# Performance work log

Hardware: AMD Instinct MI355X
Metric: run time of the kernel (lower is better)

## Reference

```python
import jax, jax.numpy as jnp
import numpy as np

B, O, N = 8, 100, 4096
TOK_D, D, K, H = 2048, 256, 128, 8
DH = D // H
LN_EPS = 1e-5


def _ln(x, g, b):
    m = x.mean(-1, keepdims=True)
    v = ((x - m) ** 2).mean(-1, keepdims=True)
    return (x - m) * jax.lax.rsqrt(v + LN_EPS) * g + b


def setup_inputs() -> dict:
    key = jax.random.key(0)
    ks = jax.random.split(key, 16)
    s = 0.02
    return {
        "activation": jax.random.uniform(ks[0], (B, O, N), jnp.float32),
        "tokens": jax.random.normal(ks[1], (B, N, TOK_D), jnp.float32),
        "W_tok": jax.random.normal(ks[2], (TOK_D, D), jnp.float32) * s,
        "b_tok": jnp.zeros((D,), jnp.float32),
        "g_tn": jnp.ones((D,), jnp.float32),
        "bt_tn": jnp.zeros((D,), jnp.float32),
        "pool_query": jax.random.normal(ks[3], (D,), jnp.float32) * s,
        "Wq": jax.random.normal(ks[4], (D, D), jnp.float32) * s,
        "bq": jnp.zeros((D,), jnp.float32),
        "Wk": jax.random.normal(ks[5], (D, D), jnp.float32) * s,
        "bk": jnp.zeros((D,), jnp.float32),
        "Wv": jax.random.normal(ks[6], (D, D), jnp.float32) * s,
        "bv": jnp.zeros((D,), jnp.float32),
        "Wo": jax.random.normal(ks[7], (D, D), jnp.float32) * s,
        "bo": jnp.zeros((D,), jnp.float32),
        "g_pn": jnp.ones((D,), jnp.float32),
        "bt_pn": jnp.zeros((D,), jnp.float32),
        "g_on": jnp.ones((D,), jnp.float32),
        "bt_on": jnp.zeros((D,), jnp.float32),
    }


def reference(activation, tokens, W_tok, b_tok, g_tn, bt_tn, pool_query,
              Wq, bq, Wk, bk, Wv, bv, Wo, bo, g_pn, bt_pn, g_on, bt_on):
    # project + norm the shared token pool: [B, N, D]
    tp = _ln(tokens @ W_tok + b_tok, g_tn, bt_tn)

    # weighted-average branch
    w = activation / jnp.clip(activation.sum(-1, keepdims=True), 1e-8)
    weighted_avg = jnp.einsum('bon,bnd->bod', w, tp)

    # top-k attention branch
    _, topk_idx = jax.lax.top_k(activation, K)            # [B, O, K]
    topk_tokens = jax.vmap(lambda t, i: t[i])(tp, topk_idx)  # [B, O, K, D]

    # MultiheadAttention with a single shared query vector (q_len = 1)
    q = (pool_query @ Wq + bq).reshape(H, DH)             # [H, DH]
    kp = (topk_tokens @ Wk + bk).reshape(B, O, K, H, DH)
    vp = (topk_tokens @ Wv + bv).reshape(B, O, K, H, DH)
    scores = jnp.einsum('hd,bokhd->bohk', q, kp) / np.sqrt(DH).astype(np.float32)
    attn = jax.nn.softmax(scores, axis=-1)                # [B, O, H, K]
    pooled = jnp.einsum('bohk,bokhd->bohd', attn, vp).reshape(B, O, D)
    pooled = _ln(pooled @ Wo + bo, g_pn, bt_pn)

    return _ln(weighted_avg + pooled, g_on, bt_on)
```

## Files before the change

### kernel.cpp

```cpp
#include <hip/hip_runtime.h>
#include <hip/hip_bf16.h>

#define DEVI static __device__ __forceinline__

typedef __attribute__((ext_vector_type(8))) short short8;
typedef __attribute__((ext_vector_type(4))) float f32x4;

#define B_   8
#define O_   100
#define N_   4096
#define TOKD 2048
#define D_   256
#define K_   128
#define H_   8
#define M_   (B_*N_)

DEVI unsigned short f2bf(float f) {
    unsigned u = __float_as_uint(f);
    u = (u + 0x7FFFu + ((u >> 16) & 1u)) >> 16;
    return (unsigned short)u;
}
DEVI float bf2f(unsigned v) { return __uint_as_float(v << 16); }

DEVI unsigned pkbf(float lo, float hi) {
    unsigned r;
    asm("v_cvt_pk_bf16_f32 %0, %1, %2" : "=v"(r) : "v"(lo), "v"(hi));
    return r;
}
DEVI void gload16(const void* g, void* l) {
    __builtin_amdgcn_global_load_lds((const __attribute__((address_space(1))) void*)g,
                                     (__attribute__((address_space(3))) void*)l, 16, 0, 0);
}

__global__ __launch_bounds__(256) void k_pre(const float* __restrict__ act,
                                             int* __restrict__ oidx,
                                             float* __restrict__ asum,
                                             const float* __restrict__ W,
                                             unsigned short* __restrict__ wtb,
                                             const float* __restrict__ pq,
                                             const float* __restrict__ Wq,
                                             const float* __restrict__ bqv,
                                             const float* __restrict__ Wk,
                                             const float* __restrict__ bkv,
                                             float* __restrict__ qW,
                                             float* __restrict__ qb) {
    __shared__ __align__(16) char smem[50304];
    const int t = threadIdx.x, lane = t & 63, wid = t >> 6;

    if (blockIdx.x >= 800) {
        const int bx = blockIdx.x - 800;
        if (bx < 2048) {
            int idx = bx * 256 + t;
            int k = idx >> 8, n = idx & 255;
            wtb[n * TOKD + k] = f2bf(W[idx]);
            return;
        }
        float (*qpart)[32] = (float(*)[32])smem;
        float* qhl = (float*)(smem + 1024);
        const int h = bx - 2048;
        const int col = h * 32 + (t & 31), sl = t >> 5;
        float s = 0.f;
        #pragma unroll
        for (int e = 0; e < 32; ++e) s += pq[sl * 32 + e] * Wq[(sl * 32 + e) * D_ + col];
        qpart[sl][t & 31] = s;
        __syncthreads();
        if (t < 32) {
            float u = bqv[h * 32 + t];
            #pragma unroll
            for (int s8 = 0; s8 < 8; ++s8) u += qpart[s8][t];
            qhl[t] = u;
        }
        __syncthreads();
        float u = 0.f;
        #pragma unroll
        for (int dd = 0; dd < 32; ++dd) u += qhl[dd] * Wk[t * D_ + h * 32 + dd];
        qW[h * D_ + t] = u;
        if (t == 0) {
            float z = 0.f;
            for (int dd = 0; dd < 32; ++dd) z += qhl[dd] * bkv[h * 32 + dd];
            qb[h] = z;
        }
        return;
    }

    int* hist = (int*)smem;
    unsigned long long* cand = (unsigned long long*)(smem + 16384);
    int* csum = (int*)(smem + 49152);
    int* sb   = (int*)(smem + 50192);
    int* cnts = (int*)(smem + 50200);
    float* redf = (float*)(smem + 50208);
    unsigned long long* redu = (unsigned long long*)(smem + 50224);

    const int blk = blockIdx.x;
    const float* rp = act + (size_t)blk * N_;
    float fv[16]; unsigned vb[16]; int bins[16];
    float fs = 0.f;
    #pragma unroll
    for (int i = 0; i < 16; ++i) {
        float f = rp[t + i * 256];
        fv[i] = f; vb[i] = __float_as_uint(f);
        fs += f;
    }
    #pragma unroll
    for (int i = 0; i < 16; ++i) hist[t + i * 256] = 0;
    if (t == 0) { cnts[0] = 0; cnts[1] = 0; }
    #pragma unroll
    for (int m = 1; m < 64; m <<= 1) fs += __shfl_xor(fs, m);
    if (!lane) redf[wid] = fs;
    __syncthreads();
    if (t == 0) asum[blk] = fmaxf(redf[0] + redf[1] + redf[2] + redf[3], 1e-8f);

    #pragma unroll
    for (int i = 0; i < 16; ++i) {
        float f = fv[i];
        int b = (f >= 1.0f) ? 4095 : ((f > 0.f) ? (int)(f * 4096.f) : 0);
        bins[i] = b;
        atomicAdd(&hist[b], 1);
    }
    __syncthreads();

    int cs = 0;
    #pragma unroll
    for (int i = 0; i < 16; ++i) cs += hist[t * 16 + i];
    int v = cs;
    #pragma unroll
    for (int off = 1; off < 64; off <<= 1) {
        int o = __shfl_down(v, off);
        if (lane + off < 64) v += o;
    }
    if (!lane) csum[256 + wid] = v;
    __syncthreads();
    int stot = 0;
    for (int w2 = wid + 1; w2 < 4; ++w2) stot += csum[256 + w2];
    int suff = v + stot;
    csum[t] = suff;
    __syncthreads();
    int nxtc = (t < 255) ? csum[t + 1] : 0;
    if (suff >= K_ && nxtc < K_) {
        int run = nxtc, bstar = t * 16;
        for (int bi = 15; bi >= 0; --bi) {
            run += hist[t * 16 + bi];
            if (run >= K_) { bstar = t * 16 + bi; break; }
        }
        sb[0] = bstar;
    }
    __syncthreads();
    const int bstar = sb[0];

    #pragma unroll
    for (int i = 0; i < 16; ++i) {
        if (bins[i] > bstar) {
            int p = atomicAdd(&cnts[0], 1);
            oidx[blk * K_ + p] = t + i * 256;
        } else if (bins[i] == bstar) {
            int p = atomicAdd(&cnts[1], 1);
            cand[p] = ((unsigned long long)vb[i] << 16) | (unsigned)(4095 - (t + i * 256));
        }
    }
    __syncthreads();
    const int g = cnts[0], E = cnts[1], m = K_ - g;
    unsigned long long last = ~0ull;
    for (int slot = 0; slot < m; ++slot) {
        unsigned long long best = 0;
        for (int i = t; i < E; i += 256) {
            unsigned long long e = cand[i];
            if (e < last && e > best) best = e;
        }
        #pragma unroll
        for (int mm = 1; mm < 64; mm <<= 1) {
            unsigned long long o = __shfl_xor(best, mm);
            if (o > best) best = o;
        }
        if (!lane) redu[wid] = best;
        __syncthreads();
        best = redu[0];
        if (redu[1] > best) best = redu[1];
        if (redu[2] > best) best = redu[2];
        if (redu[3] > best) best = redu[3];
        if (t == 0) oidx[blk * K_ + g + slot] = 4095 - (int)(best & 0xFFFFull);
        last = best;
        __syncthreads();
    }
}

__global__ __launch_bounds__(512, 2) void k_gemm1(const float* __restrict__ A,
                                                  const unsigned short* __restrict__ Bt,
                                                  const float* __restrict__ btok,
                                                  const float* __restrict__ g,
                                                  const float* __restrict__ bt,
                                                  unsigned short* __restrict__ tp) {
    __shared__ __align__(16) char smem[81920];
    const int t = threadIdx.x;
    const int bm = blockIdx.x;
    const int lane = t & 63, w = t >> 6;
    const int wm = w >> 2, wn = w & 3;
    const int lr = lane >> 4, lc = lane & 15;

    const int arow = t >> 3;
    const int acb = (t & 7) * 16;
    const float* agp = A + (size_t)(bm * 64 + arow) * TOKD + (t & 7) * 8;
    const int aw0 = arow * 128 + (acb ^ ((arow & 7) << 4));
    const unsigned short* bg = Bt + (size_t)(t >> 3) * TOKD
                        + (((((t & 7) << 4)) ^ (((t >> 3) & 7) << 4)) >> 1);
    char* bld = smem + 16384 + (w << 10);

    f32x4 acc[2][4] = {};
    const int NT = TOKD / 64;
    float4 a0, a1;

    a0 = *(const float4*)(agp); a1 = *(const float4*)(agp + 4);
    #pragma unroll
    for (int c = 0; c < 4; ++c) gload16(bg + (size_t)c * 64 * TOKD, bld + c * 8192);
    {
        uint4 v;
        v.x = pkbf(a0.x, a0.y); v.y = pkbf(a0.z, a0.w);
        v.z = pkbf(a1.x, a1.y); v.w = pkbf(a1.z, a1.w);
        *(uint4*)(smem + aw0) = v;
    }
    a0 = *(const float4*)(agp + 64); a1 = *(const float4*)(agp + 68);
    asm volatile("s_waitcnt vmcnt(2) lgkmcnt(0)" ::: "memory");
    __builtin_amdgcn_s_barrier();

    int cur = 0;
    for (int kt = 0; kt < NT; ++kt) {
        const int nxt = cur ^ 1;
        if (kt + 1 < NT) {
            const unsigned short* bn = bg + (size_t)(kt + 1) * 64;
            char* dst = bld + nxt * 32768;
            #pragma unroll
            for (int c = 0; c < 4; ++c) gload16(bn + (size_t)c * 64 * TOKD, dst + c * 8192);
        }
        const char* Ab = smem + cur * 8192;
        const char* Bb = smem + 16384 + cur * 32768;
        #pragma unroll
        for (int kk = 0; kk < 2; ++kk) {
            short8 afr[2], bfr[4];
            #pragma unroll
            for (int mi = 0; mi < 2; ++mi) {
                int row = wm * 32 + mi * 16 + lc;
                afr[mi] = *(const short8*)(Ab + row * 128 + ((kk * 64 + lr * 16) ^ ((row & 7) << 4)));
            }
            #pragma unroll
            for (int ni = 0; ni < 4; ++ni) {
                int n = wn * 64 + ni * 16 + lc;
                bfr[ni] = *(const short8*)(Bb + n * 128 + ((kk * 64 + lr * 16) ^ ((n & 7) << 4)));
            }
            __builtin_amdgcn_s_setprio(1);
            #pragma unroll
            for (int mi = 0; mi < 2; ++mi)
                #pragma unroll
                for (int ni = 0; ni < 4; ++ni)
                    acc[mi][ni] = __builtin_amdgcn_mfma_f32_16x16x32_bf16(afr[mi], bfr[ni], acc[mi][ni], 0, 0, 0);
            __builtin_amdgcn_s_setprio(0);
        }
        if (kt + 1 < NT) {
            uint4 v;
            v.x = pkbf(a0.x, a0.y); v.y = pkbf(a0.z, a0.w);
            v.z = pkbf(a1.x, a1.y); v.w = pkbf(a1.z, a1.w);
            *(uint4*)(smem + nxt * 8192 + aw0) = v;
            if (kt + 2 < NT) {
                const float* ap = agp + (size_t)(kt + 2) * 64;
                a0 = *(const float4*)(ap); a1 = *(const float4*)(ap + 4);
                asm volatile("s_waitcnt vmcnt(2) lgkmcnt(0)" ::: "memory");
            } else {
                asm volatile("s_waitcnt vmcnt(0) lgkmcnt(0)" ::: "memory");
            }
            __builtin_amdgcn_s_barrier();
            cur = nxt;
        }
    }
    __syncthreads();

    float* ep = (float*)smem;
    const int col0 = lane * 4;
    float4 b4 = *(const float4*)(btok + col0);
    float4 g4 = *(const float4*)(g + col0);
    float4 t4 = *(const float4*)(bt + col0);
    #pragma unroll
    for (int c = 0; c < 2; ++c) {
        if (wm == c) {
            #pragma unroll
            for (int mi = 0; mi < 2; ++mi)
                #pragma unroll
                for (int ni = 0; ni < 4; ++ni)
                    #pragma unroll
                    for (int r = 0; r < 4; ++r)
                        ep[(mi * 16 + lr * 4 + r) * 260 + wn * 64 + ni * 16 + lc] = acc[mi][ni][r];
        }
        __syncthreads();
        #pragma unroll
        for (int rr = 0; rr < 4; ++rr) {
            int row = w * 4 + rr;
            float4 x4 = *(const float4*)(ep + row * 260 + col0);
            float x0 = x4.x + b4.x, x1 = x4.y + b4.y, x2 = x4.z + b4.z, x3 = x4.w + b4.w;
            float s = x0 + x1 + x2 + x3;
            float q = x0*x0 + x1*x1 + x2*x2 + x3*x3;
            #pragma unroll
            for (int m = 1; m < 64; m <<= 1) { s += __shfl_xor(s, m); q += __shfl_xor(q, m); }
            float mean = s * (1.f/256.f);
            float var = q * (1.f/256.f) - mean * mean;
            float rs = rsqrtf(var + 1e-5f);
            ushort4 o;
            o.x = f2bf((x0-mean)*rs*g4.x + t4.x);
            o.y = f2bf((x1-mean)*rs*g4.y + t4.y);
            o.z = f2bf((x2-mean)*rs*g4.z + t4.z);
            o.w = f2bf((x3-mean)*rs*g4.w + t4.w);
            *(ushort4*)(tp + (size_t)(bm * 64 + c * 32 + row) * D_ + col0) = o;
        }
        __syncthreads();
    }
}

__global__ __launch_bounds__(256) void k_wavg(const float* __restrict__ act,
                                              const unsigned short* __restrict__ tp,
                                              float* __restrict__ partial) {
    const int kc = blockIdx.x;
    const int b = blockIdx.y;
    const int d = threadIdx.x;
    const unsigned short* tpb = tp + ((size_t)b * N_ + kc * 128) * D_ + d;
    const float* actb = act + (size_t)b * O_ * N_ + kc * 128;
    float* pout = partial + ((size_t)(b * 32 + kc) * O_) * D_ + d;
    for (int oci = 0; oci < 2; ++oci) {
        const int oc = blockIdx.z * 2 + oci;
        float acc[10] = {};
        #pragma unroll 2
        for (int q = 0; q < 32; ++q) {
            float t0 = bf2f(tpb[(q * 4 + 0) * D_]);
            float t1 = bf2f(tpb[(q * 4 + 1) * D_]);
            float t2 = bf2f(tpb[(q * 4 + 2) * D_]);
            float t3 = bf2f(tpb[(q * 4 + 3) * D_]);
            #pragma unroll
            for (int oj = 0; oj < 10; ++oj) {
                float4 a4 = *(const float4*)(actb + (size_t)(oc * 10 + oj) * N_ + q * 4);
                acc[oj] += a4.x * t0 + a4.y * t1 + a4.z * t2 + a4.w * t3;
            }
        }
        #pragma unroll
        for (int oj = 0; oj < 10; ++oj)
            pout[(size_t)(oc * 10 + oj) * D_] = acc[oj];
    }
}

DEVI int swz(int j, int chunk) { return j * 512 + ((chunk ^ (j & 31)) << 4); }

__global__ __launch_bounds__(256) void k_attn(
    const unsigned short* __restrict__ tp, const int* __restrict__ oidx,
    const float* __restrict__ qW, const float* __restrict__ qbv,
    const float* __restrict__ Wv, const float* __restrict__ bv,
    const float* __restrict__ Wo, const float* __restrict__ bo,
    const float* __restrict__ g_pn, const float* __restrict__ bt_pn,
    const float* __restrict__ g_on, const float* __restrict__ bt_on,
    const float* __restrict__ partial, const float* __restrict__ asum,
    float* __restrict__ outp)
{
    __shared__ uint4 tgU[4096];
    __shared__ float sc[H_ * K_];
    __shared__ float ul[H_ * D_];
    __shared__ float pool_lds[D_];
    __shared__ float redf[8];
    __shared__ int idxl[K_];
    char* tg = (char*)tgU;

    const int t = threadIdx.x, lane = t & 63, wid = t >> 6;
    const int blk = blockIdx.x;
    const int b = blk / O_;
    const int o = blk - b * O_;

    if (t < K_) idxl[t] = oidx[blk * K_ + t];
    __syncthreads();

    #pragma unroll
    for (int it = 0; it < 16; ++it) {
        int c = t + it * 256;
        int j = c >> 5, ch = c & 31;
        uint4 v = *(const uint4*)(tp + ((size_t)(b * N_ + idxl[j])) * D_ + ch * 8);
        *(uint4*)(tg + swz(j, ch)) = v;
    }
    __syncthreads();

    {
        const int j = t & 127, hq = t >> 7;
        const float* q0 = qW + hq * 4 * D_;
        float s0 = 0.f, s1 = 0.f, s2 = 0.f, s3 = 0.f;
        #pragma unroll 4
        for (int e8 = 0; e8 < 32; ++e8) {
            uint4 tv = *(const uint4*)(tg + swz(j, e8));
            float f0 = bf2f(tv.x & 0xffffu), f1 = bf2f(tv.x >> 16);
            float f2 = bf2f(tv.y & 0xffffu), f3 = bf2f(tv.y >> 16);
            float f4 = bf2f(tv.z & 0xffffu), f5 = bf2f(tv.z >> 16);
            float f6 = bf2f(tv.w & 0xffffu), f7 = bf2f(tv.w >> 16);
            const float* qa = q0 + e8 * 8;
            const float* qbp = qa + D_;
            const float* qc = qa + 2 * D_;
            const float* qd = qa + 3 * D_;
            s0 += f0*qa[0]+f1*qa[1]+f2*qa[2]+f3*qa[3]+f4*qa[4]+f5*qa[5]+f6*qa[6]+f7*qa[7];
            s1 += f0*qbp[0]+f1*qbp[1]+f2*qbp[2]+f3*qbp[3]+f4*qbp[4]+f5*qbp[5]+f6*qbp[6]+f7*qbp[7];
            s2 += f0*qc[0]+f1*qc[1]+f2*qc[2]+f3*qc[3]+f4*qc[4]+f5*qc[5]+f6*qc[6]+f7*qc[7];
            s3 += f0*qd[0]+f1*qd[1]+f2*qd[2]+f3*qd[3]+f4*qd[4]+f5*qd[5]+f6*qd[6]+f7*qd[7];
        }
        const float sca = 0.1767766952966369f;
        sc[(hq * 4 + 0) * K_ + j] = (s0 + qbv[hq * 4 + 0]) * sca;
        sc[(hq * 4 + 1) * K_ + j] = (s1 + qbv[hq * 4 + 1]) * sca;
        sc[(hq * 4 + 2) * K_ + j] = (s2 + qbv[hq * 4 + 2]) * sca;
        sc[(hq * 4 + 3) * K_ + j] = (s3 + qbv[hq * 4 + 3]) * sca;
    }
    __syncthreads();

    #pragma unroll
    for (int hh = 0; hh < 2; ++hh) {
        int h = wid * 2 + hh;
        float v0 = sc[h * K_ + lane], v1 = sc[h * K_ + 64 + lane];
        float mx = fmaxf(v0, v1);
        #pragma unroll
        for (int m = 1; m < 64; m <<= 1) mx = fmaxf(mx, __shfl_xor(mx, m));
        float e0 = __expf(v0 - mx), e1 = __expf(v1 - mx);
        float ss = e0 + e1;
        #pragma unroll
        for (int m = 1; m < 64; m <<= 1) ss += __shfl_xor(ss, m);
        float inv = 1.0f / ss;
        sc[h * K_ + lane] = e0 * inv;
        sc[h * K_ + 64 + lane] = e1 * inv;
    }
    __syncthreads();

    {
        const int h = t >> 5, eg = t & 31;
        float a8[8] = {};
        #pragma unroll 2
        for (int jb = 0; jb < 32; ++jb) {
            f32x4 p4 = *(const f32x4*)(sc + h * K_ + jb * 4);
            #pragma unroll
            for (int ji = 0; ji < 4; ++ji) {
                int j = jb * 4 + ji;
                uint4 tv = *(const uint4*)(tg + swz(j, eg));
                float pw = p4[ji];
                a8[0] += pw * bf2f(tv.x & 0xffffu); a8[1] += pw * bf2f(tv.x >> 16);
                a8[2] += pw * bf2f(tv.y & 0xffffu); a8[3] += pw * bf2f(tv.y >> 16);
                a8[4] += pw * bf2f(tv.z & 0xffffu); a8[5] += pw * bf2f(tv.z >> 16);
                a8[6] += pw * bf2f(tv.w & 0xffffu); a8[7] += pw * bf2f(tv.w >> 16);
            }
        }
        #pragma unroll
        for (int i = 0; i < 8; ++i) ul[h * D_ + eg * 8 + i] = a8[i];
    }
    __syncthreads();

    {
        int h = t >> 5;
        const float* up = ul + h * D_;
        float p = bv[t];
        #pragma unroll 8
        for (int e = 0; e < D_; ++e) p += up[e] * Wv[e * D_ + t];
        pool_lds[t] = p;
    }
    __syncthreads();
    float po = bo[t];
    #pragma unroll 8
    for (int e = 0; e < D_; ++e) po += pool_lds[e] * Wo[e * D_ + t];

    float s1 = po, q1 = po * po;
    #pragma unroll
    for (int m = 1; m < 64; m <<= 1) { s1 += __shfl_xor(s1, m); q1 += __shfl_xor(q1, m); }
    if (!lane) { redf[wid] = s1; redf[4 + wid] = q1; }
    __syncthreads();
    s1 = redf[0] + redf[1] + redf[2] + redf[3];
    q1 = redf[4] + redf[5] + redf[6] + redf[7];
    float mean = s1 * (1.f/256.f);
    float var = q1 * (1.f/256.f) - mean * mean;
    float rs = rsqrtf(var + 1e-5f);
    float pl = (po - mean) * rs * g_pn[t] + bt_pn[t];
    __syncthreads();

    float wa = 0.f;
    const float* pp = partial + ((size_t)(b * 32) * O_ + o) * D_ + t;
    #pragma unroll 8
    for (int kc = 0; kc < 32; ++kc) wa += pp[(size_t)kc * O_ * D_];
    float x = wa / asum[blk] + pl;
    float s2 = x, q2 = x * x;
    #pragma unroll
    for (int m = 1; m < 64; m <<= 1) { s2 += __shfl_xor(s2, m); q2 += __shfl_xor(q2, m); }
    if (!lane) { redf[wid] = s2; redf[4 + wid] = q2; }
    __syncthreads();
    s2 = redf[0] + redf[1] + redf[2] + redf[3];
    q2 = redf[4] + redf[5] + redf[6] + redf[7];
    float mean2 = s2 * (1.f/256.f);
    float var2 = q2 * (1.f/256.f) - mean2 * mean2;
    float rs2 = rsqrtf(var2 + 1e-5f);
    outp[(size_t)blk * D_ + t] = (x - mean2) * rs2 * g_on[t] + bt_on[t];
}

extern "C" void kernel_launch(void* const* d_in, const int* in_sizes, int n_in,
                              void* d_out, int out_size, void* d_ws, size_t ws_size,
                              hipStream_t stream) {
    const float* act    = (const float*)d_in[0];
    const float* tokens = (const float*)d_in[1];
    const float* W_tok  = (const float*)d_in[2];
    const float* b_tok  = (const float*)d_in[3];
    const float* g_tn   = (const float*)d_in[4];
    const float* bt_tn  = (const float*)d_in[5];
    const float* pq     = (const float*)d_in[6];
    const float* Wq     = (const float*)d_in[7];
    const float* bq     = (const float*)d_in[8];
    const float* Wk     = (const float*)d_in[9];
    const float* bk     = (const float*)d_in[10];
    const float* Wv     = (const float*)d_in[11];
    const float* bv     = (const float*)d_in[12];
    const float* Wo     = (const float*)d_in[13];
    const float* bo     = (const float*)d_in[14];
    const float* g_pn   = (const float*)d_in[15];
    const float* bt_pn  = (const float*)d_in[16];
    const float* g_on   = (const float*)d_in[17];
    const float* bt_on  = (const float*)d_in[18];

    char* ws = (char*)d_ws;
    unsigned short* wtb   = (unsigned short*)ws;
    unsigned short* tp    = (unsigned short*)(ws + 1048576);
    int*   tidx = (int*)(ws + 17825792);
    float* asum = (float*)(ws + 18235392);
    float* part = (float*)(ws + 18238592);
    float* qW   = (float*)(ws + 44452992);
    float* qb   = (float*)(ws + 44461184);

    k_pre<<<2856, 256, 0, stream>>>(act, tidx, asum, W_tok, wtb,
                                    pq, Wq, bq, Wk, bk, qW, qb);
    k_gemm1<<<M_ / 64, 512, 0, stream>>>(tokens, wtb, b_tok, g_tn, bt_tn, tp);
    k_wavg<<<dim3(32, 8, 5), 256, 0, stream>>>(act, tp, part);
    k_attn<<<B_ * O_, 256, 0, stream>>>(tp, tidx, qW, qb, Wv, bv, Wo, bo,
                                        g_pn, bt_pn, g_on, bt_on, part, asum,
                                        (float*)d_out);
}
```

Baseline: 221.6 us.

## Load GEMM operands directly into registers instead of staging through LDS

The token-projection GEMM kernel stops staging A and B tiles through shared memory with double-buffered global_load_lds. Each wave now loads its MFMA fragments straight from global memory into registers, prefetching two k-steps ahead. This removes the per-iteration barriers and LDS traffic, and LDS use shrinks to the epilogue buffer. In exchange, operand reuse across waves is lost, so global and L2 traffic rises and register pressure grows; the launch bound also drops the two-blocks-per-CU hint.

```diff
diff --git a/kernel.cpp b/kernel.cpp
--- a/kernel.cpp
+++ b/kernel.cpp
@@ -27,9 +27,11 @@
     asm("v_cvt_pk_bf16_f32 %0, %1, %2" : "=v"(r) : "v"(lo), "v"(hi));
     return r;
 }
-DEVI void gload16(const void* g, void* l) {
-    __builtin_amdgcn_global_load_lds((const __attribute__((address_space(1))) void*)g,
-                                     (__attribute__((address_space(3))) void*)l, 16, 0, 0);
+DEVI short8 pack8(float4 x, float4 y) {
+    union { unsigned u[4]; short8 s; } r;
+    r.u[0] = pkbf(x.x, x.y); r.u[1] = pkbf(x.z, x.w);
+    r.u[2] = pkbf(y.x, y.y); r.u[3] = pkbf(y.z, y.w);
+    return r.s;
 }
 
 __global__ __launch_bounds__(256) void k_pre(const float* __restrict__ act,
@@ -183,99 +185,90 @@
     }
 }
 
-__global__ __launch_bounds__(512, 2) void k_gemm1(const float* __restrict__ A,
-                                                  const unsigned short* __restrict__ Bt,
-                                                  const float* __restrict__ btok,
-                                                  const float* __restrict__ g,
-                                                  const float* __restrict__ bt,
-                                                  unsigned short* __restrict__ tp) {
-    __shared__ __align__(16) char smem[81920];
+#define GBODY(KT, BCUR)                                                                          \
+    {                                                                                            \
+        _Pragma("unroll")                                                                        \
+        for (int mi = 0; mi < 2; ++mi)                                                           \
+            _Pragma("unroll")                                                                    \
+            for (int ni = 0; ni < 4; ++ni) {                                                     \
+                acc[mi][ni] = __builtin_amdgcn_mfma_f32_16x16x32_bf16(ab[mi*2+0], BCUR[ni*2+0], acc[mi][ni], 0, 0, 0); \
+                acc[mi][ni] = __builtin_amdgcn_mfma_f32_16x16x32_bf16(ab[mi*2+1], BCUR[ni*2+1], acc[mi][ni], 0, 0, 0); \
+            }                                                                                    \
+        ab[0] = pack8(t00, t01); ab[1] = pack8(t02, t03);                                        \
+        ab[2] = pack8(t10, t11); ab[3] = pack8(t12, t13);                                        \
+        if ((KT) + 2 < NT) {                                                                     \
+            const float* ap0 = a0p + ((KT) + 2) * 64;                                            \
+            const float* ap1 = a1p + ((KT) + 2) * 64;                                            \
+            t00 = *(const float4*)(ap0);      t01 = *(const float4*)(ap0 + 4);                   \
+            t02 = *(const float4*)(ap0 + 32); t03 = *(const float4*)(ap0 + 36);                  \
+            t10 = *(const float4*)(ap1);      t11 = *(const float4*)(ap1 + 4);                   \
+            t12 = *(const float4*)(ap1 + 32); t13 = *(const float4*)(ap1 + 36);                  \
+            const unsigned short* q0 = b0p + ((KT) + 2) * 64;                                    \
+            const unsigned short* q1 = b1p + ((KT) + 2) * 64;                                    \
+            const unsigned short* q2 = b2p + ((KT) + 2) * 64;                                    \
+            const unsigned short* q3 = b3p + ((KT) + 2) * 64;                                    \
+            BCUR[0] = *(const short8*)(q0); BCUR[1] = *(const short8*)(q0 + 32);                 \
+            BCUR[2] = *(const short8*)(q1); BCUR[3] = *(const short8*)(q1 + 32);                 \
+            BCUR[4] = *(const short8*)(q2); BCUR[5] = *(const short8*)(q2 + 32);                 \
+            BCUR[6] = *(const short8*)(q3); BCUR[7] = *(const short8*)(q3 + 32);                 \
+        }                                                                                        \
+    }
+
+__global__ __launch_bounds__(512) void k_gemm1(const float* __restrict__ A,
+                                               const unsigned short* __restrict__ Bt,
+                                               const float* __restrict__ btok,
+                                               const float* __restrict__ g,
+                                               const float* __restrict__ bt,
+                                               unsigned short* __restrict__ tp) {
+    __shared__ __align__(16) float ep[32 * 260];
     const int t = threadIdx.x;
     const int bm = blockIdx.x;
     const int lane = t & 63, w = t >> 6;
     const int wm = w >> 2, wn = w & 3;
     const int lr = lane >> 4, lc = lane & 15;
-
-    const int arow = t >> 3;
-    const int acb = (t & 7) * 16;
-    const float* agp = A + (size_t)(bm * 64 + arow) * TOKD + (t & 7) * 8;
-    const int aw0 = arow * 128 + (acb ^ ((arow & 7) << 4));
-    const unsigned short* bg = Bt + (size_t)(t >> 3) * TOKD
-                        + (((((t & 7) << 4)) ^ (((t >> 3) & 7) << 4)) >> 1);
-    char* bld = smem + 16384 + (w << 10);
+    const int NT = TOKD / 64;
+
+    const float* a0p = A + (size_t)(bm * 64 + wm * 32 + lc) * TOKD + lr * 8;
+    const float* a1p = a0p + (size_t)16 * TOKD;
+    const unsigned short* b0p = Bt + (size_t)(wn * 64 + lc) * TOKD + lr * 8;
+    const unsigned short* b1p = b0p + (size_t)16 * TOKD;
+    const unsigned short* b2p = b0p + (size_t)32 * TOKD;
+    const unsigned short* b3p = b0p + (size_t)48 * TOKD;
 
     f32x4 acc[2][4] = {};
-    const int NT = TOKD / 64;
-    float4 a0, a1;
-
-    a0 = *(const float4*)(agp); a1 = *(const float4*)(agp + 4);
-    #pragma unroll
-    for (int c = 0; c < 4; ++c) gload16(bg + (size_t)c * 64 * TOKD, bld + c * 8192);
-    {
-        uint4 v;
-        v.x = pkbf(a0.x, a0.y); v.y = pkbf(a0.z, a0.w);
-        v.z = pkbf(a1.x, a1.y); v.w = pkbf(a1.z, a1.w);
-        *(uint4*)(smem + aw0) = v;
-    }
-    a0 = *(const float4*)(agp + 64); a1 = *(const float4*)(agp + 68);
-    asm volatile("s_waitcnt vmcnt(2) lgkmcnt(0)" ::: "memory");
-    __builtin_amdgcn_s_barrier();
-
-    int cur = 0;
-    for (int kt = 0; kt < NT; ++kt) {
-        const int nxt = cur ^ 1;
-        if (kt + 1 < NT) {
-            const unsigned short* bn = bg + (size_t)(kt + 1) * 64;
-            char* dst = bld + nxt * 32768;
-            #pragma unroll
-            for (int c = 0; c < 4; ++c) gload16(bn + (size_t)c * 64 * TOKD, dst + c * 8192);
-        }
-        const char* Ab = smem + cur * 8192;
-        const char* Bb = smem + 16384 + cur * 32768;
-        #pragma unroll
-        for (int kk = 0; kk < 2; ++kk) {
-            short8 afr[2], bfr[4];
-            #pragma unroll
-            for (int mi = 0; mi < 2; ++mi) {
-                int row = wm * 32 + mi * 16 + lc;
-                afr[mi] = *(const short8*)(Ab + row * 128 + ((kk * 64 + lr * 16) ^ ((row & 7) << 4)));
-            }
-            #pragma unroll
-            for (int ni = 0; ni < 4; ++ni) {
-                int n = wn * 64 + ni * 16 + lc;
-                bfr[ni] = *(const short8*)(Bb + n * 128 + ((kk * 64 + lr * 16) ^ ((n & 7) << 4)));
-            }
-            __builtin_amdgcn_s_setprio(1);
-            #pragma unroll
-            for (int mi = 0; mi < 2; ++mi)
-                #pragma unroll
-                for (int ni = 0; ni < 4; ++ni)
-                    acc[mi][ni] = __builtin_amdgcn_mfma_f32_16x16x32_bf16(afr[mi], bfr[ni], acc[mi][ni], 0, 0, 0);
-            __builtin_amdgcn_s_setprio(0);
-        }
-        if (kt + 1 < NT) {
-            uint4 v;
-            v.x = pkbf(a0.x, a0.y); v.y = pkbf(a0.z, a0.w);
-            v.z = pkbf(a1.x, a1.y); v.w = pkbf(a1.z, a1.w);
-            *(uint4*)(smem + nxt * 8192 + aw0) = v;
-            if (kt + 2 < NT) {
-                const float* ap = agp + (size_t)(kt + 2) * 64;
-                a0 = *(const float4*)(ap); a1 = *(const float4*)(ap + 4);
-                asm volatile("s_waitcnt vmcnt(2) lgkmcnt(0)" ::: "memory");
-            } else {
-                asm volatile("s_waitcnt vmcnt(0) lgkmcnt(0)" ::: "memory");
-            }
-            __builtin_amdgcn_s_barrier();
-            cur = nxt;
-        }
-    }
-    __syncthreads();
-
-    float* ep = (float*)smem;
+    short8 bS0[8], bS1[8];
+    short8 ab[4];
+    float4 t00, t01, t02, t03, t10, t11, t12, t13;
+
+    t00 = *(const float4*)(a0p);      t01 = *(const float4*)(a0p + 4);
+    t02 = *(const float4*)(a0p + 32); t03 = *(const float4*)(a0p + 36);
+    t10 = *(const float4*)(a1p);      t11 = *(const float4*)(a1p + 4);
+    t12 = *(const float4*)(a1p + 32); t13 = *(const float4*)(a1p + 36);
+    bS0[0] = *(const short8*)(b0p);      bS0[1] = *(const short8*)(b0p + 32);
+    bS0[2] = *(const short8*)(b1p);      bS0[3] = *(const short8*)(b1p + 32);
+    bS0[4] = *(const short8*)(b2p);      bS0[5] = *(const short8*)(b2p + 32);
+    bS0[6] = *(const short8*)(b3p);      bS0[7] = *(const short8*)(b3p + 32);
+    bS1[0] = *(const short8*)(b0p + 64); bS1[1] = *(const short8*)(b0p + 96);
+    bS1[2] = *(const short8*)(b1p + 64); bS1[3] = *(const short8*)(b1p + 96);
+    bS1[4] = *(const short8*)(b2p + 64); bS1[5] = *(const short8*)(b2p + 96);
+    bS1[6] = *(const short8*)(b3p + 64); bS1[7] = *(const short8*)(b3p + 96);
+    ab[0] = pack8(t00, t01); ab[1] = pack8(t02, t03);
+    ab[2] = pack8(t10, t11); ab[3] = pack8(t12, t13);
+    t00 = *(const float4*)(a0p + 64);  t01 = *(const float4*)(a0p + 68);
+    t02 = *(const float4*)(a0p + 96);  t03 = *(const float4*)(a0p + 100);
+    t10 = *(const float4*)(a1p + 64);  t11 = *(const float4*)(a1p + 68);
+    t12 = *(const float4*)(a1p + 96);  t13 = *(const float4*)(a1p + 100);
+
+    for (int kt = 0; kt < NT; kt += 2) {
+        GBODY(kt, bS0)
+        GBODY(kt + 1, bS1)
+    }
+
     const int col0 = lane * 4;
     float4 b4 = *(const float4*)(btok + col0);
     float4 g4 = *(const float4*)(g + col0);
     float4 t4 = *(const float4*)(bt + col0);
+    __syncthreads();
     #pragma unroll
     for (int c = 0; c < 2; ++c) {
         if (wm == c) {
```

Result: slower. 392.1 us (+77.0%).

## Split pre-kernel, tile weight transpose via LDS, halve attention LDS footprint

Applied to the files above, without the earlier changes.

Moves the W_tok bf16 transpose into its own kernel that stages 256x32 tiles in LDS, so writes to the transposed weight are coalesced instead of scattered element stores. The top-k/query-fold work becomes a separate kernel launched after the weighted-average kernel. The attention kernel now gathers the 128 top-k token rows in two halves of 64 and reuses that buffer for the ul and pool scratch, roughly halving LDS use to allow more resident blocks, at the cost of gathering each half twice across the score and value passes. The Wv and Wo matvecs gain four independent accumulators for more ILP.

```diff
diff --git a/kernel.cpp b/kernel.cpp
--- a/kernel.cpp
+++ b/kernel.cpp
@@ -32,32 +32,45 @@
                                      (__attribute__((address_space(3))) void*)l, 16, 0, 0);
 }
 
-__global__ __launch_bounds__(256) void k_pre(const float* __restrict__ act,
-                                             int* __restrict__ oidx,
-                                             float* __restrict__ asum,
-                                             const float* __restrict__ W,
-                                             unsigned short* __restrict__ wtb,
-                                             const float* __restrict__ pq,
-                                             const float* __restrict__ Wq,
-                                             const float* __restrict__ bqv,
-                                             const float* __restrict__ Wk,
-                                             const float* __restrict__ bkv,
-                                             float* __restrict__ qW,
-                                             float* __restrict__ qb) {
+__global__ __launch_bounds__(256) void k_trans(const float* __restrict__ W,
+                                               unsigned short* __restrict__ wtb) {
+    __shared__ unsigned short ldsT[32 * 264];
+    const int t = threadIdx.x;
+    const int k0 = (blockIdx.x >> 3) * 256;
+    const int n0 = (blockIdx.x & 7) * 32;
+    const int nn = t & 31, kk8 = t >> 5;
+    #pragma unroll
+    for (int r = 0; r < 32; ++r) {
+        int k = r * 8 + kk8;
+        ldsT[nn * 264 + k] = f2bf(W[(size_t)(k0 + k) * D_ + n0 + nn]);
+    }
+    __syncthreads();
+    const int w = t >> 6, l = t & 63;
+    #pragma unroll
+    for (int rr = 0; rr < 8; ++rr) {
+        int n = w * 8 + rr;
+        ushort4 v = *(const ushort4*)(&ldsT[n * 264 + l * 4]);
+        *(ushort4*)(wtb + (size_t)(n0 + n) * TOKD + k0 + l * 4) = v;
+    }
+}
+
+__global__ __launch_bounds__(256) void k_topkqf(const float* __restrict__ act,
+                                                int* __restrict__ oidx,
+                                                float* __restrict__ asum,
+                                                const float* __restrict__ pq,
+                                                const float* __restrict__ Wq,
+                                                const float* __restrict__ bqv,
+                                                const float* __restrict__ Wk,
+                                                const float* __restrict__ bkv,
+                                                float* __restrict__ qW,
+                                                float* __restrict__ qb) {
     __shared__ __align__(16) char smem[50304];
     const int t = threadIdx.x, lane = t & 63, wid = t >> 6;
 
     if (blockIdx.x >= 800) {
-        const int bx = blockIdx.x - 800;
-        if (bx < 2048) {
-            int idx = bx * 256 + t;
-            int k = idx >> 8, n = idx & 255;
-            wtb[n * TOKD + k] = f2bf(W[idx]);
-            return;
-        }
         float (*qpart)[32] = (float(*)[32])smem;
         float* qhl = (float*)(smem + 1024);
-        const int h = bx - 2048;
+        const int h = blockIdx.x - 800;
         const int col = h * 32 + (t & 31), sl = t >> 5;
         float s = 0.f;
         #pragma unroll
@@ -341,7 +354,7 @@
     }
 }
 
-DEVI int swz(int j, int chunk) { return j * 512 + ((chunk ^ (j & 31)) << 4); }
+DEVI int swz64(int j, int chunk) { return j * 512 + ((chunk ^ (j & 31)) << 4); }
 
 __global__ __launch_bounds__(256) void k_attn(
     const unsigned short* __restrict__ tp, const int* __restrict__ oidx,
@@ -353,13 +366,12 @@
     const float* __restrict__ partial, const float* __restrict__ asum,
     float* __restrict__ outp)
 {
-    __shared__ uint4 tgU[4096];
+    __shared__ __align__(16) char tg[32768];
     __shared__ float sc[H_ * K_];
-    __shared__ float ul[H_ * D_];
-    __shared__ float pool_lds[D_];
     __shared__ float redf[8];
     __shared__ int idxl[K_];
-    char* tg = (char*)tgU;
+    float* ul = (float*)tg;
+    float* pool_lds = (float*)(tg + 8192);
 
     const int t = threadIdx.x, lane = t & 63, wid = t >> 6;
     const int blk = blockIdx.x;
@@ -369,42 +381,37 @@
     if (t < K_) idxl[t] = oidx[blk * K_ + t];
     __syncthreads();
 
-    #pragma unroll
-    for (int it = 0; it < 16; ++it) {
-        int c = t + it * 256;
-        int j = c >> 5, ch = c & 31;
-        uint4 v = *(const uint4*)(tp + ((size_t)(b * N_ + idxl[j])) * D_ + ch * 8);
-        *(uint4*)(tg + swz(j, ch)) = v;
-    }
-    __syncthreads();
-
-    {
-        const int j = t & 127, hq = t >> 7;
-        const float* q0 = qW + hq * 4 * D_;
-        float s0 = 0.f, s1 = 0.f, s2 = 0.f, s3 = 0.f;
+    const int jq = t & 63, hp = t >> 6;
+    const float* qr0 = qW + (hp * 2) * D_;
+    const float* qr1 = qr0 + D_;
+    const float sca = 0.1767766952966369f;
+
+    for (int pass = 0; pass < 2; ++pass) {
+        #pragma unroll
+        for (int it = 0; it < 8; ++it) {
+            int c = t + it * 256;
+            int j = c >> 5, ch = c & 31;
+            uint4 v = *(const uint4*)(tp + ((size_t)(b * N_ + idxl[pass * 64 + j])) * D_ + ch * 8);
+            *(uint4*)(tg + swz64(j, ch)) = v;
+        }
+        __syncthreads();
+        float s0 = 0.f, s1 = 0.f;
         #pragma unroll 4
         for (int e8 = 0; e8 < 32; ++e8) {
-            uint4 tv = *(const uint4*)(tg + swz(j, e8));
+            uint4 tv = *(const uint4*)(tg + swz64(jq, e8));
             float f0 = bf2f(tv.x & 0xffffu), f1 = bf2f(tv.x >> 16);
             float f2 = bf2f(tv.y & 0xffffu), f3 = bf2f(tv.y >> 16);
             float f4 = bf2f(tv.z & 0xffffu), f5 = bf2f(tv.z >> 16);
             float f6 = bf2f(tv.w & 0xffffu), f7 = bf2f(tv.w >> 16);
-            const float* qa = q0 + e8 * 8;
-            const float* qbp = qa + D_;
-            const float* qc = qa + 2 * D_;
-            const float* qd = qa + 3 * D_;
+            const float* qa = qr0 + e8 * 8;
+            const float* qc = qr1 + e8 * 8;
             s0 += f0*qa[0]+f1*qa[1]+f2*qa[2]+f3*qa[3]+f4*qa[4]+f5*qa[5]+f6*qa[6]+f7*qa[7];
-            s1 += f0*qbp[0]+f1*qbp[1]+f2*qbp[2]+f3*qbp[3]+f4*qbp[4]+f5*qbp[5]+f6*qbp[6]+f7*qbp[7];
-            s2 += f0*qc[0]+f1*qc[1]+f2*qc[2]+f3*qc[3]+f4*qc[4]+f5*qc[5]+f6*qc[6]+f7*qc[7];
-            s3 += f0*qd[0]+f1*qd[1]+f2*qd[2]+f3*qd[3]+f4*qd[4]+f5*qd[5]+f6*qd[6]+f7*qd[7];
-        }
-        const float sca = 0.1767766952966369f;
-        sc[(hq * 4 + 0) * K_ + j] = (s0 + qbv[hq * 4 + 0]) * sca;
-        sc[(hq * 4 + 1) * K_ + j] = (s1 + qbv[hq * 4 + 1]) * sca;
-        sc[(hq * 4 + 2) * K_ + j] = (s2 + qbv[hq * 4 + 2]) * sca;
-        sc[(hq * 4 + 3) * K_ + j] = (s3 + qbv[hq * 4 + 3]) * sca;
-    }
-    __syncthreads();
+            s1 += f0*qc[0]+f1*qc[1]+f2*qc[2]+f3*qc[3]+f4*qc[4]+f5*qc[5]+f6*qc[6]+f7*qc[7];
+        }
+        sc[(hp * 2)     * K_ + pass * 64 + jq] = (s0 + qbv[hp * 2])     * sca;
+        sc[(hp * 2 + 1) * K_ + pass * 64 + jq] = (s1 + qbv[hp * 2 + 1]) * sca;
+        __syncthreads();
+    }
 
     #pragma unroll
     for (int hh = 0; hh < 2; ++hh) {
@@ -423,50 +430,86 @@
     }
     __syncthreads();
 
-    {
-        const int h = t >> 5, eg = t & 31;
-        float a8[8] = {};
-        #pragma unroll 2
-        for (int jb = 0; jb < 32; ++jb) {
-            f32x4 p4 = *(const f32x4*)(sc + h * K_ + jb * 4);
-            #pragma unroll
-            for (int ji = 0; ji < 4; ++ji) {
-                int j = jb * 4 + ji;
-                uint4 tv = *(const uint4*)(tg + swz(j, eg));
-                float pw = p4[ji];
-                a8[0] += pw * bf2f(tv.x & 0xffffu); a8[1] += pw * bf2f(tv.x >> 16);
-                a8[2] += pw * bf2f(tv.y & 0xffffu); a8[3] += pw * bf2f(tv.y >> 16);
-                a8[4] += pw * bf2f(tv.z & 0xffffu); a8[5] += pw * bf2f(tv.z >> 16);
-                a8[6] += pw * bf2f(tv.w & 0xffffu); a8[7] += pw * bf2f(tv.w >> 16);
-            }
-        }
-        #pragma unroll
-        for (int i = 0; i < 8; ++i) ul[h * D_ + eg * 8 + i] = a8[i];
-    }
+    const int hq5 = t >> 5, eg = t & 31;
+    float a8[8] = {};
+    #pragma unroll 2
+    for (int jb = 0; jb < 16; ++jb) {
+        f32x4 p4 = *(const f32x4*)(sc + hq5 * K_ + 64 + jb * 4);
+        #pragma unroll
+        for (int ji = 0; ji < 4; ++ji) {
+            int j = jb * 4 + ji;
+            uint4 tv = *(const uint4*)(tg + swz64(j, eg));
+            float pw = p4[ji];
+            a8[0] += pw * bf2f(tv.x & 0xffffu); a8[1] += pw * bf2f(tv.x >> 16);
+            a8[2] += pw * bf2f(tv.y & 0xffffu); a8[3] += pw * bf2f(tv.y >> 16);
+            a8[4] += pw * bf2f(tv.z & 0xffffu); a8[5] += pw * bf2f(tv.z >> 16);
+            a8[6] += pw * bf2f(tv.w & 0xffffu); a8[7] += pw * bf2f(tv.w >> 16);
+        }
+    }
+    __syncthreads();
+    #pragma unroll
+    for (int it = 0; it < 8; ++it) {
+        int c = t + it * 256;
+        int j = c >> 5, ch = c & 31;
+        uint4 v = *(const uint4*)(tp + ((size_t)(b * N_ + idxl[j])) * D_ + ch * 8);
+        *(uint4*)(tg + swz64(j, ch)) = v;
+    }
+    __syncthreads();
+    #pragma unroll 2
+    for (int jb = 0; jb < 16; ++jb) {
+        f32x4 p4 = *(const f32x4*)(sc + hq5 * K_ + jb * 4);
+        #pragma unroll
+        for (int ji = 0; ji < 4; ++ji) {
+            int j = jb * 4 + ji;
+            uint4 tv = *(const uint4*)(tg + swz64(j, eg));
+            float pw = p4[ji];
+            a8[0] += pw * bf2f(tv.x & 0xffffu); a8[1] += pw * bf2f(tv.x >> 16);
+            a8[2] += pw * bf2f(tv.y & 0xffffu); a8[3] += pw * bf2f(tv.y >> 16);
+            a8[4] += pw * bf2f(tv.z & 0xffffu); a8[5] += pw * bf2f(tv.z >> 16);
+            a8[6] += pw * bf2f(tv.w & 0xffffu); a8[7] += pw * bf2f(tv.w >> 16);
+        }
+    }
+    __syncthreads();
+    #pragma unroll
+    for (int i = 0; i < 8; ++i) ul[hq5 * D_ + eg * 8 + i] = a8[i];
     __syncthreads();
 
     {
         int h = t >> 5;
         const float* up = ul + h * D_;
-        float p = bv[t];
-        #pragma unroll 8
-        for (int e = 0; e < D_; ++e) p += up[e] * Wv[e * D_ + t];
-        pool_lds[t] = p;
-    }
-    __syncthreads();
-    float po = bo[t];
-    #pragma unroll 8
-    for (int e = 0; e < D_; ++e) po += pool_lds[e] * Wo[e * D_ + t];
-
-    float s1 = po, q1 = po * po;
-    #pragma unroll
-    for (int m = 1; m < 64; m <<= 1) { s1 += __shfl_xor(s1, m); q1 += __shfl_xor(q1, m); }
-    if (!lane) { redf[wid] = s1; redf[4 + wid] = q1; }
-    __syncthreads();
-    s1 = redf[0] + redf[1] + redf[2] + redf[3];
-    q1 = redf[4] + redf[5] + redf[6] + redf[7];
-    float mean = s1 * (1.f/256.f);
-    float var = q1 * (1.f/256.f) - mean * mean;
+        float p0 = 0.f, p1 = 0.f, p2 = 0.f, p3 = 0.f;
+        #pragma unroll 4
+        for (int e = 0; e < 64; ++e) {
+            p0 += up[e]       * Wv[(size_t)e         * D_ + t];
+            p1 += up[e + 64]  * Wv[(size_t)(e + 64)  * D_ + t];
+            p2 += up[e + 128] * Wv[(size_t)(e + 128) * D_ + t];
+            p3 += up[e + 192] * Wv[(size_t)(e + 192) * D_ + t];
+        }
+        pool_lds[t] = bv[t] + ((p0 + p1) + (p2 + p3));
+    }
+    __syncthreads();
+    float po;
+    {
+        float p0 = 0.f, p1 = 0.f, p2 = 0.f, p3 = 0.f;
+        #pragma unroll 4
+        for (int e = 0; e < 64; ++e) {
+            p0 += pool_lds[e]       * Wo[(size_t)e         * D_ + t];
+            p1 += pool_lds[e + 64]  * Wo[(size_t)(e + 64)  * D_ + t];
+            p2 += pool_lds[e + 128] * Wo[(size_t)(e + 128) * D_ + t];
+            p3 += pool_lds[e + 192] * Wo[(size_t)(e + 192) * D_ + t];
+        }
+        po = bo[t] + ((p0 + p1) + (p2 + p3));
+    }
+
+    float lsm = po, lqm = po * po;
+    #pragma unroll
+    for (int m = 1; m < 64; m <<= 1) { lsm += __shfl_xor(lsm, m); lqm += __shfl_xor(lqm, m); }
+    if (!lane) { redf[wid] = lsm; redf[4 + wid] = lqm; }
+    __syncthreads();
+    lsm = redf[0] + redf[1] + redf[2] + redf[3];
+    lqm = redf[4] + redf[5] + redf[6] + redf[7];
+    float mean = lsm * (1.f/256.f);
+    float var = lqm * (1.f/256.f) - mean * mean;
     float rs = rsqrtf(var + 1e-5f);
     float pl = (po - mean) * rs * g_pn[t] + bt_pn[t];
     __syncthreads();
@@ -521,10 +564,10 @@
     float* qW   = (float*)(ws + 44452992);
     float* qb   = (float*)(ws + 44461184);
 
-    k_pre<<<2856, 256, 0, stream>>>(act, tidx, asum, W_tok, wtb,
-                                    pq, Wq, bq, Wk, bk, qW, qb);
+    k_trans<<<64, 256, 0, stream>>>(W_tok, wtb);
     k_gemm1<<<M_ / 64, 512, 0, stream>>>(tokens, wtb, b_tok, g_tn, bt_tn, tp);
     k_wavg<<<dim3(32, 8, 5), 256, 0, stream>>>(act, tp, part);
+    k_topkqf<<<808, 256, 0, stream>>>(act, tidx, asum, pq, Wq, bq, Wk, bk, qW, qb);
     k_attn<<<B_ * O_, 256, 0, stream>>>(tp, tidx, qW, qb, Wv, bv, Wo, bo,
                                         g_pn, bt_pn, g_on, bt_on, part, asum,
                                         (float*)d_out);
```

New measurement: 219.5 us (median of 2 runs). Within noise of the previous version (-0.9%).
